# Kernel tuning notes

Hardware: AMD Instinct MI355X
Metric: run time of the kernel (lower is better)

The kernel has to match this reference:

```python
import jax, jax.numpy as jnp
import numpy as np

DIM = 1024
N_HEADS = 16
HEAD_DIM = DIM // N_HEADS


def setup_inputs() -> dict:
    key = jax.random.key(0)
    ks = jax.random.split(key, 9)
    s = 0.02
    return {
        "x": jax.random.normal(ks[0], (2, 2048, DIM), dtype=jnp.float32),
        "Wq": jax.random.normal(ks[1], (DIM, DIM), dtype=jnp.float32) * s,
        "bq": jax.random.normal(ks[2], (DIM,), dtype=jnp.float32) * s,
        "Wk": jax.random.normal(ks[3], (DIM, DIM), dtype=jnp.float32) * s,
        "bk": jax.random.normal(ks[4], (DIM,), dtype=jnp.float32) * s,
        "Wv": jax.random.normal(ks[5], (DIM, DIM), dtype=jnp.float32) * s,
        "bv": jax.random.normal(ks[6], (DIM,), dtype=jnp.float32) * s,
        "Wo": jax.random.normal(ks[7], (DIM, DIM), dtype=jnp.float32) * s,
        "bo": jax.random.normal(ks[8], (DIM,), dtype=jnp.float32) * s,
    }


def reference(x, Wq, bq, Wk, bk, Wv, bv, Wo, bo):
    B, T, C = x.shape
    # QKV projections, split heads -> [B, H, T, D]
    def split_heads(t):
        return t.reshape(B, T, N_HEADS, HEAD_DIM).transpose(0, 2, 1, 3)
    q = split_heads(x @ Wq + bq)
    k = split_heads(x @ Wk + bk)
    v = split_heads(x @ Wv + bv)
    scale = 1.0 / jnp.sqrt(jnp.float32(HEAD_DIM))
    scores = jnp.einsum("bhqd,bhkd->bhqk", q, k) * scale  # [B,H,T,T]
    causal = jnp.tril(jnp.ones((T, T), dtype=bool))  # True = keep
    scores = jnp.where(causal, scores, jnp.float32(-jnp.inf))
    weights = jax.nn.softmax(scores, axis=-1)
    ctx = jnp.einsum("bhqk,bhkd->bhqd", weights, v)
    ctx = ctx.transpose(0, 2, 1, 3).reshape(B, T, C)
    return ctx @ Wo + bo
```

## Files before the change

kernel.cpp:

```cpp
#include <hip/hip_runtime.h>
#include <hip/hip_bf16.h>
#include <stdint.h>

#define DIM    1024
#define SEQ    2048
#define NB     2
#define NH     16
#define HD     64
#define NROWS  (NB*SEQ)

typedef unsigned short u16;
typedef __attribute__((ext_vector_type(8))) short bf16x8;
typedef __attribute__((ext_vector_type(4))) float f32x4;
typedef __attribute__((ext_vector_type(4))) unsigned short u16x4;

#define NEG_INF (-__builtin_inff())

__device__ __forceinline__ u16 f2bf(float f) {
    union { float f; uint32_t u; } x; x.f = f;
    uint32_t r = x.u + 0x7FFFu + ((x.u >> 16) & 1u);
    return (u16)(r >> 16);
}

__device__ __forceinline__ uint32_t cvtpk(float a, float b) {
    uint32_t r;
    asm volatile("v_cvt_pk_bf16_f32 %0, %1, %2" : "=v"(r) : "v"(a), "v"(b));
    return r;
}

__device__ __forceinline__ void gload_lds16(const void* g, void* l) {
    __builtin_amdgcn_global_load_lds(
        (const __attribute__((address_space(1))) void*)g,
        (__attribute__((address_space(3))) void*)l, 16, 0, 0);
}

__global__ __launch_bounds__(256)
void cvt_x(const float* __restrict__ in, u16* __restrict__ out)
{
    size_t i = (size_t)blockIdx.x * 256 + threadIdx.x;
    float4 f = *(const float4*)&in[i * 4];
    u16x4 o = { f2bf(f.x), f2bf(f.y), f2bf(f.z), f2bf(f.w) };
    *(u16x4*)&out[i * 4] = o;
}

__global__ __launch_bounds__(256)
void cvt_w(const float* __restrict__ Wq, const float* __restrict__ Wk,
           const float* __restrict__ Wv, const float* __restrict__ Wo,
           u16* __restrict__ Wqt, u16* __restrict__ Wkt,
           u16* __restrict__ Wvt, u16* __restrict__ Wot)
{
    __shared__ u16 Ws[64][68];
    const int z = blockIdx.z;
    const float* W = z == 0 ? Wq : z == 1 ? Wk : z == 2 ? Wv : Wo;
    u16* Wt        = z == 0 ? Wqt : z == 1 ? Wkt : z == 2 ? Wvt : Wot;
    const int k0 = blockIdx.x * 64;
    const int n0 = blockIdx.y * 64;
    const int tid = threadIdx.x;

    #pragma unroll
    for (int it = 0; it < 4; ++it) {
        int idx = tid + it * 256;
        int r = idx >> 4, cq = idx & 15;
        float4 f = *(const float4*)&W[(size_t)(k0 + r) * DIM + n0 + cq * 4];
        u16x4 o = { f2bf(f.x), f2bf(f.y), f2bf(f.z), f2bf(f.w) };
        *(u16x4*)&Ws[r][cq * 4] = o;
    }
    __syncthreads();
    #pragma unroll
    for (int it = 0; it < 4; ++it) {
        int idx = tid + it * 256;
        int rr = idx >> 4, cq = idx & 15;
        u16x4 o = { Ws[cq*4+0][rr], Ws[cq*4+1][rr], Ws[cq*4+2][rr], Ws[cq*4+3][rr] };
        *(u16x4*)&Wt[(size_t)(n0 + rr) * DIM + k0 + cq * 4] = o;
    }
}

template<int MODE>
__global__ __launch_bounds__(256)
void gemm_mfma(const u16* __restrict__ A,
               const u16* __restrict__ Wt0, const u16* __restrict__ Wt1,
               const u16* __restrict__ Wt2,
               const float* __restrict__ b0, const float* __restrict__ b1,
               const float* __restrict__ b2,
               void* __restrict__ o0, void* __restrict__ o1, void* __restrict__ o2)
{
    __shared__ __align__(16) uint8_t lds[32768];
    uint8_t* Asb = lds;
    uint8_t* Bsb = lds + 16384;

    const int tid  = threadIdx.x;
    const int wid  = tid >> 6, lane = tid & 63;
    const int lr   = lane & 15, lg = lane >> 4;
    const int wr   = wid >> 1, wc = wid & 1;

    const int r0 = blockIdx.x * 128;
    const int c0 = blockIdx.y * 128;

    const u16* Wt; const float* bias; u16* obf = nullptr; float* ofp = nullptr;
    int cw; float qscale = 1.0f;
    if (MODE == 0) {
        int sel = c0 >> 10;
        cw  = c0 & 1023;
        Wt   = sel == 0 ? Wt0 : sel == 1 ? Wt1 : Wt2;
        bias = sel == 0 ? b0  : sel == 1 ? b1  : b2;
        obf  = (u16*)(sel == 0 ? o0 : sel == 1 ? o1 : o2);
        if (sel == 0) qscale = 0.125f * 1.44269504088896f;
    } else {
        cw = c0; Wt = Wt0; bias = b0; ofp = (float*)o0;
    }

    f32x4 acc[4][4] = {};

    for (int k0 = 0; k0 < DIM; k0 += 64) {
        __syncthreads();
        #pragma unroll
        for (int seg = 0; seg < 4; ++seg) {
            int o   = seg * 4096 + tid * 16;
            int row = o >> 7;
            int sch = ((o >> 4) & 7) ^ (row & 7);
            gload_lds16((const uint8_t*)A  + ((size_t)(r0 + row) << 11) + (k0 << 1) + (sch << 4),
                        Asb + seg * 4096 + (wid << 10) + (lane << 4));
            gload_lds16((const uint8_t*)Wt + ((size_t)(cw + row) << 11) + (k0 << 1) + (sch << 4),
                        Bsb + seg * 4096 + (wid << 10) + (lane << 4));
        }
        __syncthreads();

        __builtin_amdgcn_s_setprio(1);
        #pragma unroll
        for (int kk = 0; kk < 2; ++kk) {
            bf16x8 a[4], b[4];
            #pragma unroll
            for (int i = 0; i < 4; ++i) {
                int ar = wr * 64 + i * 16 + lr;
                a[i] = *(const bf16x8*)(Asb + ar * 128 + ((((kk << 2) | lg) ^ (ar & 7)) << 4));
                int br = wc * 64 + i * 16 + lr;
                b[i] = *(const bf16x8*)(Bsb + br * 128 + ((((kk << 2) | lg) ^ (br & 7)) << 4));
            }
            #pragma unroll
            for (int i = 0; i < 4; ++i)
                #pragma unroll
                for (int j = 0; j < 4; ++j)
                    acc[i][j] = __builtin_amdgcn_mfma_f32_16x16x32_bf16(a[i], b[j], acc[i][j], 0, 0, 0);
        }
        __builtin_amdgcn_s_setprio(0);
    }

    #pragma unroll
    for (int j = 0; j < 4; ++j) {
        int colw = wc * 64 + j * 16 + lr;
        float bv = bias[cw + colw];
        #pragma unroll
        for (int i = 0; i < 4; ++i) {
            #pragma unroll
            for (int r = 0; r < 4; ++r) {
                float val = (acc[i][j][r] + bv) * qscale;
                int row = r0 + wr * 64 + i * 16 + lg * 4 + r;
                if (MODE == 0) {
                    int col = cw + colw;
                    int h = col >> 6, d = col & 63;
                    int bb = row >> 11, t = row & (SEQ - 1);
                    obf[((((size_t)bb * NH + h) * SEQ + t) << 6) + d] = f2bf(val);
                } else {
                    ofp[((size_t)row << 10) + c0 + colw] = val;
                }
            }
        }
    }
}

template<int SPLIT>
__global__ __launch_bounds__(256)
void attn_mfma(const u16* __restrict__ q, const u16* __restrict__ k,
               const u16* __restrict__ v, u16* __restrict__ ctx,
               float* __restrict__ pO, float* __restrict__ pML)
{
    __shared__ __align__(16) uint8_t lds[16384];
    uint8_t* Ks = lds;
    uint8_t* Vt = lds + 8192;

    const int tid = threadIdx.x;
    const int wid = tid >> 6, lane = tid & 63;
    const int lr  = lane & 15, lg = lane >> 4;

    const int n = blockIdx.x;
    int bh, qt, k_lo, k_hi, pidx = 0;
    if (SPLIT) {
        bh = n & 31;
        int u = n >> 5;
        qt = u >> 1;
        int chunk = u & 1;
        int T = qt + 1, hh = (T + 1) >> 1;
        k_lo = chunk ? hh : 0;
        k_hi = chunk ? T : hh;
        pidx = (((bh << 5) | qt) << 1) | chunk;
    } else {
        int j4 = n >> 8, c = n & 255, ch = c >> 5;
        bh = c & 31;
        qt = (j4 == 0) ? ch : (j4 == 1) ? (15 - ch)
           : (j4 == 2) ? (16 + ch) : (31 - ch);
        k_lo = 0; k_hi = qt + 1;
    }

    const size_t hb = (size_t)bh * SEQ * HD;
    const int q0 = qt * 64;

    const u16* qrow = q + hb + ((size_t)(q0 + wid * 16 + lr) << 6);
    bf16x8 aQ0 = *(const bf16x8*)(qrow + lg * 8);
    bf16x8 aQ1 = *(const bf16x8*)(qrow + 32 + lg * 8);

    const int kr  = tid >> 2;
    const int kc0 = (tid & 3) * 2;
    const u16* kbase = k + hb + ((size_t)kr << 6) + kc0 * 8;

    const int vp = tid >> 3;
    const int vg = tid & 7;
    const int vj  = vp >> 3;
    const int vlg = (vp >> 1) & 3;
    const int vrr = (vp & 1) * 2;
    const int vslot = (vj & 1) * 32 + vlg * 8 + ((vj >> 1) << 2) + vrr;
    const u16* vbase = v + hb + ((size_t)(2 * vp) << 6) + vg * 8;

    bf16x8 kpre0 = {}, kpre1 = {}, vpre0 = {}, vpre1 = {};
    if (k_lo < k_hi) {
        const u16* ks = kbase + ((size_t)k_lo << 12);
        kpre0 = *(const bf16x8*)(ks);
        kpre1 = *(const bf16x8*)(ks + 8);
        const u16* vs = vbase + ((size_t)k_lo << 12);
        vpre0 = *(const bf16x8*)(vs);
        vpre1 = *(const bf16x8*)(vs + 64);
    }

    f32x4 acc[4] = {};
    float m_own = NEG_INF;
    float l_own = 0.f;

    for (int kt = k_lo; kt < k_hi; ++kt) {
        __syncthreads();
        *(bf16x8*)(Ks + kr * 128 + ((kc0       ^ (kr & 7)) << 4)) = kpre0;
        *(bf16x8*)(Ks + kr * 128 + (((kc0 + 1) ^ (kr & 7)) << 4)) = kpre1;
        #pragma unroll
        for (int i = 0; i < 8; ++i) {
            int d = vg * 8 + i;
            int swzd = (d ^ (d >> 3)) & 7;
            uint32_t w = (uint32_t)(u16)vpre0[i] | ((uint32_t)(u16)vpre1[i] << 16);
            *(uint32_t*)(Vt + d * 128 + ((((vslot >> 3) ^ swzd) << 4))
                         + ((vslot & 7) << 1)) = w;
        }
        __syncthreads();

        if (kt + 1 < k_hi) {
            const u16* ks = kbase + ((size_t)(kt + 1) << 12);
            kpre0 = *(const bf16x8*)(ks);
            kpre1 = *(const bf16x8*)(ks + 8);
            const u16* vs = vbase + ((size_t)(kt + 1) << 12);
            vpre0 = *(const bf16x8*)(vs);
            vpre1 = *(const bf16x8*)(vs + 64);
        }

        f32x4 s[4];
        __builtin_amdgcn_s_setprio(1);
        #pragma unroll
        for (int j = 0; j < 4; ++j) {
            int krow = j * 16 + lr;
            bf16x8 b0 = *(const bf16x8*)(Ks + krow * 128 + ((lg       ^ (krow & 7)) << 4));
            bf16x8 b1 = *(const bf16x8*)(Ks + krow * 128 + (((4 | lg) ^ (krow & 7)) << 4));
            f32x4 z = {0.f, 0.f, 0.f, 0.f};
            z    = __builtin_amdgcn_mfma_f32_16x16x32_bf16(b0, aQ0, z, 0, 0, 0);
            s[j] = __builtin_amdgcn_mfma_f32_16x16x32_bf16(b1, aQ1, z, 0, 0, 0);
        }
        __builtin_amdgcn_s_setprio(0);

        if (kt == qt) {
            #pragma unroll
            for (int j = 0; j < 4; ++j)
                #pragma unroll
                for (int r = 0; r < 4; ++r)
                    if (j * 16 + lg * 4 + r > wid * 16 + lr) s[j][r] = NEG_INF;
        }

        float rm = NEG_INF;
        #pragma unroll
        for (int j = 0; j < 4; ++j) {
            float a = fmaxf(fmaxf(s[j][0], s[j][1]), fmaxf(s[j][2], s[j][3]));
            rm = fmaxf(rm, a);
        }
        rm = fmaxf(rm, __shfl_xor(rm, 16));
        rm = fmaxf(rm, __shfl_xor(rm, 32));

        if (!__all(rm <= m_own + 8.f)) {
            float mnew = fmaxf(m_own, rm);
            float aown = exp2f(m_own - mnew);
            m_own = mnew;
            l_own *= aown;
            float ar[4];
            #pragma unroll
            for (int r = 0; r < 4; ++r) ar[r] = __shfl(aown, lg * 4 + r);
            #pragma unroll
            for (int ni = 0; ni < 4; ++ni)
                #pragma unroll
                for (int r = 0; r < 4; ++r)
                    acc[ni][r] *= ar[r];
        }

        float rs = 0.f;
        #pragma unroll
        for (int j = 0; j < 4; ++j)
            #pragma unroll
            for (int r = 0; r < 4; ++r) {
                float p = exp2f(s[j][r] - m_own);
                s[j][r] = p;
                rs += p;
            }
        rs += __shfl_xor(rs, 16);
        rs += __shfl_xor(rs, 32);
        l_own += rs;

        union { uint32_t u[4]; bf16x8 h; } P0, P1;
        P0.u[0] = cvtpk(s[0][0], s[0][1]); P0.u[1] = cvtpk(s[0][2], s[0][3]);
        P0.u[2] = cvtpk(s[2][0], s[2][1]); P0.u[3] = cvtpk(s[2][2], s[2][3]);
        P1.u[0] = cvtpk(s[1][0], s[1][1]); P1.u[1] = cvtpk(s[1][2], s[1][3]);
        P1.u[2] = cvtpk(s[3][0], s[3][1]); P1.u[3] = cvtpk(s[3][2], s[3][3]);

        __builtin_amdgcn_s_setprio(1);
        #pragma unroll
        for (int ni = 0; ni < 4; ++ni) {
            int vrow = ni * 16 + lr;
            int swzd = (vrow ^ (vrow >> 3)) & 7;
            bf16x8 vb0 = *(const bf16x8*)(Vt + vrow * 128 + ((lg       ^ swzd) << 4));
            bf16x8 vb1 = *(const bf16x8*)(Vt + vrow * 128 + (((4 | lg) ^ swzd) << 4));
            acc[ni] = __builtin_amdgcn_mfma_f32_16x16x32_bf16(P0.h, vb0, acc[ni], 0, 0, 0);
            acc[ni] = __builtin_amdgcn_mfma_f32_16x16x32_bf16(P1.h, vb1, acc[ni], 0, 0, 0);
        }
        __builtin_amdgcn_s_setprio(0);
    }

    if (SPLIT) {
        float* Op = pO + (size_t)pidx * 4096;
        #pragma unroll
        for (int r = 0; r < 4; ++r) {
            int row = wid * 16 + lg * 4 + r;
            #pragma unroll
            for (int ni = 0; ni < 4; ++ni)
                Op[row * 64 + ni * 16 + lr] = acc[ni][r];
        }
        if (lg == 0) {
            pML[pidx * 128 + wid * 16 + lr]      = m_own;
            pML[pidx * 128 + 64 + wid * 16 + lr] = l_own;
        }
    } else {
        float rinv = 1.f / l_own;
        float rl[4];
        #pragma unroll
        for (int r = 0; r < 4; ++r) rl[r] = __shfl(rinv, lg * 4 + r);
        const int b = bh >> 4, h = bh & 15;
        #pragma unroll
        for (int r = 0; r < 4; ++r) {
            int t = q0 + wid * 16 + lg * 4 + r;
            size_t base = (((size_t)b * SEQ + t) << 10) + (h << 6);
            #pragma unroll
            for (int ni = 0; ni < 4; ++ni)
                ctx[base + ni * 16 + lr] = f2bf(acc[ni][r] * rl[r]);
        }
    }
}

__global__ __launch_bounds__(256)
void attn_combine(const float* __restrict__ pO, const float* __restrict__ pML,
                  u16* __restrict__ ctx)
{
    int gid  = blockIdx.x * 256 + threadIdx.x;
    int rg   = gid >> 2;
    int dseg = gid & 3;
    int bh = rg >> 11;
    int qt = (rg >> 6) & 31;
    int r  = rg & 63;
    int p0 = ((bh << 5) | qt) << 1;

    float m0 = pML[p0 * 128 + r],       l0 = pML[p0 * 128 + 64 + r];
    float m1 = pML[(p0 + 1) * 128 + r], l1 = pML[(p0 + 1) * 128 + 64 + r];
    float m  = fmaxf(m0, m1);
    float s0 = exp2f(m0 - m), s1 = exp2f(m1 - m);
    float rl = 1.f / (l0 * s0 + l1 * s1);

    const float* O0 = pO + (size_t)p0 * 4096 + r * 64 + dseg * 16;
    const float* O1 = O0 + 4096;

    int b = bh >> 4, h = bh & 15, t = qt * 64 + r;
    u16* dst = ctx + (((size_t)b * SEQ + t) << 10) + (h << 6) + dseg * 16;

    u16x4 o[4];
    #pragma unroll
    for (int i = 0; i < 4; ++i) {
        float4 a = *(const float4*)&O0[i * 4];
        float4 c = *(const float4*)&O1[i * 4];
        o[i].x = f2bf((a.x * s0 + c.x * s1) * rl);
        o[i].y = f2bf((a.y * s0 + c.y * s1) * rl);
        o[i].z = f2bf((a.z * s0 + c.z * s1) * rl);
        o[i].w = f2bf((a.w * s0 + c.w * s1) * rl);
    }
    *(u16x4*)(dst)      = o[0];
    *(u16x4*)(dst + 4)  = o[1];
    *(u16x4*)(dst + 8)  = o[2];
    *(u16x4*)(dst + 12) = o[3];
}

extern "C" void kernel_launch(void* const* d_in, const int* in_sizes, int n_in,
                              void* d_out, int out_size, void* d_ws, size_t ws_size,
                              hipStream_t stream)
{
    (void)in_sizes; (void)n_in; (void)out_size;
    const float* x  = (const float*)d_in[0];
    const float* Wq = (const float*)d_in[1];
    const float* bq = (const float*)d_in[2];
    const float* Wk = (const float*)d_in[3];
    const float* bk = (const float*)d_in[4];
    const float* Wv = (const float*)d_in[5];
    const float* bv = (const float*)d_in[6];
    const float* Wo = (const float*)d_in[7];
    const float* bo = (const float*)d_in[8];

    u16* ws = (u16*)d_ws;
    const size_t M1 = (size_t)1024 * 1024;
    const size_t M4 = (size_t)NROWS * DIM;
    u16* xb  = ws;
    u16* wqt = ws + M4;
    u16* wkt = wqt + M1;
    u16* wvt = wkt + M1;
    u16* wot = wvt + M1;
    u16* qb  = wot + M1;
    u16* kb  = qb + M4;
    u16* vb  = kb + M4;
    u16* cb  = vb + M4;
    float* pO  = (float*)(cb + M4);
    float* pML = pO + (size_t)2048 * 4096;

    const size_t need = (size_t)(cb + M4 - ws) * 2
                      + (size_t)2048 * 4096 * 4 + (size_t)2048 * 128 * 4;
    const bool split = ws_size >= need;

    cvt_x<<<dim3(4096), dim3(256), 0, stream>>>(x, xb);
    cvt_w<<<dim3(16, 16, 4), dim3(256), 0, stream>>>(Wq, Wk, Wv, Wo, wqt, wkt, wvt, wot);
    gemm_mfma<0><<<dim3(32, 24), dim3(256), 0, stream>>>(
        xb, wqt, wkt, wvt, bq, bk, bv, qb, kb, vb);
    if (split) {
        attn_mfma<1><<<dim3(2048), dim3(256), 0, stream>>>(qb, kb, vb, nullptr, pO, pML);
        attn_combine<<<dim3(1024), dim3(256), 0, stream>>>(pO, pML, cb);
    } else {
        attn_mfma<0><<<dim3(1024), dim3(256), 0, stream>>>(qb, kb, vb, cb, nullptr, nullptr);
    }
    gemm_mfma<1><<<dim3(32, 8), dim3(256), 0, stream>>>(
        cb, wot, nullptr, nullptr, bo, nullptr, nullptr, d_out, nullptr, nullptr);
}
```

Before: 191.3 us.

## Pre-transpose V and read K/V tiles directly from global memory in attention

Adds a kernel that writes V in [bh, d, t] layout into the now-unused x buffer. The attention kernel drops its LDS staging, swizzling and both block barriers, and each wave loads its K and transposed V fragments straight from global memory. This is meant to remove barrier stalls and LDS write traffic. The cost is redundant global and L2 reads across the four waves, non-prefetched loads, and an extra launch. Block-index mapping also changes, removing the load-balancing qt permutation in favour of qt-major ordering.

```diff
diff --git a/kernel.cpp b/kernel.cpp
--- a/kernel.cpp
+++ b/kernel.cpp
@@ -11,6 +11,7 @@
 
 typedef unsigned short u16;
 typedef __attribute__((ext_vector_type(8))) short bf16x8;
+typedef __attribute__((ext_vector_type(4))) short bf16x4;
 typedef __attribute__((ext_vector_type(4))) float f32x4;
 typedef __attribute__((ext_vector_type(4))) unsigned short u16x4;
 
@@ -73,6 +74,34 @@
         u16x4 o = { Ws[cq*4+0][rr], Ws[cq*4+1][rr], Ws[cq*4+2][rr], Ws[cq*4+3][rr] };
         *(u16x4*)&Wt[(size_t)(n0 + rr) * DIM + k0 + cq * 4] = o;
     }
+}
+
+__global__ __launch_bounds__(256)
+void cvt_vt(const u16* __restrict__ vb, u16* __restrict__ vbt)
+{
+    __shared__ u16 T[64][65];
+    const int tid = threadIdx.x;
+    const int t0  = blockIdx.x * 64;
+    const size_t hb = (size_t)blockIdx.y << 17;
+
+    const int r  = tid >> 2;
+    const int c0 = (tid & 3) * 16;
+    const u16* src = vb + hb + ((size_t)(t0 + r) << 6) + c0;
+    bf16x8 v0 = *(const bf16x8*)src;
+    bf16x8 v1 = *(const bf16x8*)(src + 8);
+    #pragma unroll
+    for (int i = 0; i < 8; ++i) {
+        T[r][c0 + i]     = (u16)v0[i];
+        T[r][c0 + 8 + i] = (u16)v1[i];
+    }
+    __syncthreads();
+    const int d = tid >> 2;
+    u16 tmp[16];
+    #pragma unroll
+    for (int i = 0; i < 16; ++i) tmp[i] = T[c0 + i][d];
+    u16* dst = vbt + hb + ((size_t)d << 11) + t0 + c0;
+    *(bf16x8*)dst       = *(bf16x8*)&tmp[0];
+    *(bf16x8*)(dst + 8) = *(bf16x8*)&tmp[8];
 }
 
 template<int MODE>
@@ -171,13 +200,9 @@
 template<int SPLIT>
 __global__ __launch_bounds__(256)
 void attn_mfma(const u16* __restrict__ q, const u16* __restrict__ k,
-               const u16* __restrict__ v, u16* __restrict__ ctx,
+               const u16* __restrict__ vt, u16* __restrict__ ctx,
                float* __restrict__ pO, float* __restrict__ pML)
 {
-    __shared__ __align__(16) uint8_t lds[16384];
-    uint8_t* Ks = lds;
-    uint8_t* Vt = lds + 8192;
-
     const int tid = threadIdx.x;
     const int wid = tid >> 6, lane = tid & 63;
     const int lr  = lane & 15, lg = lane >> 4;
@@ -185,90 +210,56 @@
     const int n = blockIdx.x;
     int bh, qt, k_lo, k_hi, pidx = 0;
     if (SPLIT) {
-        bh = n & 31;
-        int u = n >> 5;
-        qt = u >> 1;
-        int chunk = u & 1;
+        qt = n >> 6; bh = (n >> 1) & 31;
+        int chunk = n & 1;
         int T = qt + 1, hh = (T + 1) >> 1;
         k_lo = chunk ? hh : 0;
         k_hi = chunk ? T : hh;
         pidx = (((bh << 5) | qt) << 1) | chunk;
     } else {
-        int j4 = n >> 8, c = n & 255, ch = c >> 5;
-        bh = c & 31;
-        qt = (j4 == 0) ? ch : (j4 == 1) ? (15 - ch)
-           : (j4 == 2) ? (16 + ch) : (31 - ch);
+        qt = n >> 5; bh = n & 31;
         k_lo = 0; k_hi = qt + 1;
     }
 
-    const size_t hb = (size_t)bh * SEQ * HD;
+    const size_t hb = (size_t)bh << 17;
     const int q0 = qt * 64;
 
     const u16* qrow = q + hb + ((size_t)(q0 + wid * 16 + lr) << 6);
     bf16x8 aQ0 = *(const bf16x8*)(qrow + lg * 8);
     bf16x8 aQ1 = *(const bf16x8*)(qrow + 32 + lg * 8);
 
-    const int kr  = tid >> 2;
-    const int kc0 = (tid & 3) * 2;
-    const u16* kbase = k + hb + ((size_t)kr << 6) + kc0 * 8;
-
-    const int vp = tid >> 3;
-    const int vg = tid & 7;
-    const int vj  = vp >> 3;
-    const int vlg = (vp >> 1) & 3;
-    const int vrr = (vp & 1) * 2;
-    const int vslot = (vj & 1) * 32 + vlg * 8 + ((vj >> 1) << 2) + vrr;
-    const u16* vbase = v + hb + ((size_t)(2 * vp) << 6) + vg * 8;
-
-    bf16x8 kpre0 = {}, kpre1 = {}, vpre0 = {}, vpre1 = {};
-    if (k_lo < k_hi) {
-        const u16* ks = kbase + ((size_t)k_lo << 12);
-        kpre0 = *(const bf16x8*)(ks);
-        kpre1 = *(const bf16x8*)(ks + 8);
-        const u16* vs = vbase + ((size_t)k_lo << 12);
-        vpre0 = *(const bf16x8*)(vs);
-        vpre1 = *(const bf16x8*)(vs + 64);
-    }
-
     f32x4 acc[4] = {};
     float m_own = NEG_INF;
     float l_own = 0.f;
 
     for (int kt = k_lo; kt < k_hi; ++kt) {
-        __syncthreads();
-        *(bf16x8*)(Ks + kr * 128 + ((kc0       ^ (kr & 7)) << 4)) = kpre0;
-        *(bf16x8*)(Ks + kr * 128 + (((kc0 + 1) ^ (kr & 7)) << 4)) = kpre1;
-        #pragma unroll
-        for (int i = 0; i < 8; ++i) {
-            int d = vg * 8 + i;
-            int swzd = (d ^ (d >> 3)) & 7;
-            uint32_t w = (uint32_t)(u16)vpre0[i] | ((uint32_t)(u16)vpre1[i] << 16);
-            *(uint32_t*)(Vt + d * 128 + ((((vslot >> 3) ^ swzd) << 4))
-                         + ((vslot & 7) << 1)) = w;
-        }
-        __syncthreads();
-
-        if (kt + 1 < k_hi) {
-            const u16* ks = kbase + ((size_t)(kt + 1) << 12);
-            kpre0 = *(const bf16x8*)(ks);
-            kpre1 = *(const bf16x8*)(ks + 8);
-            const u16* vs = vbase + ((size_t)(kt + 1) << 12);
-            vpre0 = *(const bf16x8*)(vs);
-            vpre1 = *(const bf16x8*)(vs + 64);
-        }
+        const u16* kb_t = k  + hb + ((size_t)kt << 12);
+        const u16* vt_t = vt + hb + kt * 64;
 
         f32x4 s[4];
         __builtin_amdgcn_s_setprio(1);
         #pragma unroll
         for (int j = 0; j < 4; ++j) {
-            int krow = j * 16 + lr;
-            bf16x8 b0 = *(const bf16x8*)(Ks + krow * 128 + ((lg       ^ (krow & 7)) << 4));
-            bf16x8 b1 = *(const bf16x8*)(Ks + krow * 128 + (((4 | lg) ^ (krow & 7)) << 4));
+            const u16* krp = kb_t + ((j * 16 + lr) << 6);
+            bf16x8 b0 = *(const bf16x8*)(krp + lg * 8);
+            bf16x8 b1 = *(const bf16x8*)(krp + 32 + lg * 8);
             f32x4 z = {0.f, 0.f, 0.f, 0.f};
             z    = __builtin_amdgcn_mfma_f32_16x16x32_bf16(b0, aQ0, z, 0, 0, 0);
             s[j] = __builtin_amdgcn_mfma_f32_16x16x32_bf16(b1, aQ1, z, 0, 0, 0);
         }
         __builtin_amdgcn_s_setprio(0);
+
+        bf16x8 vb0[4], vb1[4];
+        #pragma unroll
+        for (int ni = 0; ni < 4; ++ni) {
+            const u16* vr = vt_t + ((size_t)(ni * 16 + lr) << 11) + lg * 4;
+            bf16x4 a0 = *(const bf16x4*)(vr);
+            bf16x4 c0 = *(const bf16x4*)(vr + 16);
+            bf16x4 a1 = *(const bf16x4*)(vr + 32);
+            bf16x4 c1 = *(const bf16x4*)(vr + 48);
+            vb0[ni] = bf16x8{a0[0],a0[1],a0[2],a0[3], a1[0],a1[1],a1[2],a1[3]};
+            vb1[ni] = bf16x8{c0[0],c0[1],c0[2],c0[3], c1[0],c1[1],c1[2],c1[3]};
+        }
 
         if (kt == qt) {
             #pragma unroll
@@ -324,12 +315,8 @@
         __builtin_amdgcn_s_setprio(1);
         #pragma unroll
         for (int ni = 0; ni < 4; ++ni) {
-            int vrow = ni * 16 + lr;
-            int swzd = (vrow ^ (vrow >> 3)) & 7;
-            bf16x8 vb0 = *(const bf16x8*)(Vt + vrow * 128 + ((lg       ^ swzd) << 4));
-            bf16x8 vb1 = *(const bf16x8*)(Vt + vrow * 128 + (((4 | lg) ^ swzd) << 4));
-            acc[ni] = __builtin_amdgcn_mfma_f32_16x16x32_bf16(P0.h, vb0, acc[ni], 0, 0, 0);
-            acc[ni] = __builtin_amdgcn_mfma_f32_16x16x32_bf16(P1.h, vb1, acc[ni], 0, 0, 0);
+            acc[ni] = __builtin_amdgcn_mfma_f32_16x16x32_bf16(P0.h, vb0[ni], acc[ni], 0, 0, 0);
+            acc[ni] = __builtin_amdgcn_mfma_f32_16x16x32_bf16(P1.h, vb1[ni], acc[ni], 0, 0, 0);
         }
         __builtin_amdgcn_s_setprio(0);
     }
@@ -442,11 +429,12 @@
     cvt_w<<<dim3(16, 16, 4), dim3(256), 0, stream>>>(Wq, Wk, Wv, Wo, wqt, wkt, wvt, wot);
     gemm_mfma<0><<<dim3(32, 24), dim3(256), 0, stream>>>(
         xb, wqt, wkt, wvt, bq, bk, bv, qb, kb, vb);
+    cvt_vt<<<dim3(32, 32), dim3(256), 0, stream>>>(vb, xb);
     if (split) {
-        attn_mfma<1><<<dim3(2048), dim3(256), 0, stream>>>(qb, kb, vb, nullptr, pO, pML);
+        attn_mfma<1><<<dim3(2048), dim3(256), 0, stream>>>(qb, kb, xb, nullptr, pO, pML);
         attn_combine<<<dim3(1024), dim3(256), 0, stream>>>(pO, pML, cb);
     } else {
-        attn_mfma<0><<<dim3(1024), dim3(256), 0, stream>>>(qb, kb, vb, cb, nullptr, nullptr);
+        attn_mfma<0><<<dim3(1024), dim3(256), 0, stream>>>(qb, kb, xb, cb, nullptr, nullptr);
     }
     gemm_mfma<1><<<dim3(32, 8), dim3(256), 0, stream>>>(
         cb, wot, nullptr, nullptr, bo, nullptr, nullptr, d_out, nullptr, nullptr);
```

Result: slower. 341.6 us (+78.5%).
